# Performance work log

Measured on AMD Instinct MI355X. Metric: run time of the kernel, lower is better.

Reference implementation:

```python
import jax, jax.numpy as jnp
import numpy as np
from jax import lax

# --- model/problem dims (see init_kwargs) ---
G, NPG, R, F, HID, L = 40, 500, 8, 256, 256, 3   # graphs(frames), nodes/graph, relations, feat, hidden, layers
N = G * NPG                                       # 20000 nodes
EPG = 8000
E = G * EPG                                       # 320000 edges
TOTAL = L * HID                                   # 768 = concat of layer outputs
LSTM_IN, LSTM_HID, NCLASS = 256, 256, 2
RATIO = 0.5
K = int(np.ceil(RATIO * NPG))                     # 250 nodes kept per graph by SAGPool


def setup_inputs() -> dict:
    key = jax.random.key(0)
    ks = jax.random.split(key, 16)
    s = 0.05
    x = jax.random.normal(ks[0], (N, F), dtype=jnp.float32)
    # intra-graph edges: node ids offset by graph index
    off = jnp.arange(G, dtype=jnp.int32)[:, None] * NPG
    src = jax.random.randint(ks[1], (G, EPG), 0, NPG, dtype=jnp.int32) + off
    dst = jax.random.randint(ks[2], (G, EPG), 0, NPG, dtype=jnp.int32) + off
    edge_index = jnp.stack([src.reshape(-1), dst.reshape(-1)])
    edge_attr = jax.random.randint(ks[3], (E,), 0, R, dtype=jnp.int32)
    batch = jnp.repeat(jnp.arange(G, dtype=jnp.int32), NPG)
    # RGCN layer params (layer0 in=F==HID so all layers stack)
    conv_W = jax.random.normal(ks[4], (L, R, HID, HID), dtype=jnp.float32) * s
    conv_root = jax.random.normal(ks[5], (L, HID, HID), dtype=jnp.float32) * s
    conv_bias = jnp.zeros((L, HID), dtype=jnp.float32)
    # SAGPool scorer: RGCNConv(TOTAL, 1, R)
    pool_W = jax.random.normal(ks[6], (R, TOTAL, 1), dtype=jnp.float32) * s
    pool_root = jax.random.normal(ks[7], (TOTAL, 1), dtype=jnp.float32) * s
    pool_bias = jnp.zeros((1,), dtype=jnp.float32)
    fc1_W = jax.random.normal(ks[8], (LSTM_IN, TOTAL), dtype=jnp.float32) * s
    fc1_b = jnp.zeros((LSTM_IN,), dtype=jnp.float32)
    W_ih = jax.random.normal(ks[9], (4 * LSTM_HID, LSTM_IN), dtype=jnp.float32) * s
    W_hh = jax.random.normal(ks[10], (4 * LSTM_HID, LSTM_HID), dtype=jnp.float32) * s
    b_ih = jnp.zeros((4 * LSTM_HID,), dtype=jnp.float32)
    b_hh = jnp.zeros((4 * LSTM_HID,), dtype=jnp.float32)
    fc2_W = jax.random.normal(ks[11], (NCLASS, LSTM_HID), dtype=jnp.float32) * s
    fc2_b = jnp.zeros((NCLASS,), dtype=jnp.float32)
    return dict(x=x, edge_index=edge_index, edge_attr=edge_attr, batch=batch,
                conv_W=conv_W, conv_root=conv_root, conv_bias=conv_bias,
                pool_W=pool_W, pool_root=pool_root, pool_bias=pool_bias,
                fc1_W=fc1_W, fc1_b=fc1_b, W_ih=W_ih, W_hh=W_hh, b_ih=b_ih, b_hh=b_hh,
                fc2_W=fc2_W, fc2_b=fc2_b)


def rgcn_conv(x, src, dst, etype, W, root, bias):
    """PyG (Fast)RGCNConv: per-relation mean aggregation summed over relations + root + bias."""
    num_nodes = x.shape[0]
    Rr = W.shape[0]
    h_all = jnp.einsum('ni,rio->rno', x, W)          # [R, N, out] per-relation transform
    msg = h_all[etype, src]                           # [E, out] per-edge message
    seg = dst * Rr + etype                            # (node, relation) segment id
    cnt = jax.ops.segment_sum(jnp.ones((src.shape[0],), x.dtype), seg,
                              num_segments=num_nodes * Rr)
    norm = 1.0 / jnp.maximum(cnt[seg], 1.0)           # per-(dst,rel) mean normalization
    agg = jax.ops.segment_sum(msg * norm[:, None], dst, num_segments=num_nodes)
    return agg + x @ root + bias


def lstm_scan(xs, W_ih, W_hh, b_ih, b_hh):
    """torch.nn.LSTM (single layer, batch=1) over sequence xs [T, in]; torch gate order i,f,g,o."""
    H = W_hh.shape[1]
    def step(carry, xt):
        h, c = carry
        gates = xt @ W_ih.T + h @ W_hh.T + b_ih + b_hh
        i, f, g, o = jnp.split(gates, 4)
        c = jax.nn.sigmoid(f) * c + jax.nn.sigmoid(i) * jnp.tanh(g)
        h = jax.nn.sigmoid(o) * jnp.tanh(c)
        return (h, c), h
    init = (jnp.zeros((H,), xs.dtype), jnp.zeros((H,), xs.dtype))
    (h, c), ys = lax.scan(step, init, xs)
    return ys, h


def reference(x, edge_index, edge_attr, batch,
              conv_W, conv_root, conv_bias,
              pool_W, pool_root, pool_bias,
              fc1_W, fc1_b, W_ih, W_hh, b_ih, b_hh, fc2_W, fc2_b):
    src, dst = edge_index[0], edge_index[1]
    # stacked RGCN layers, outputs concatenated (dropout omitted: eval mode)
    h = x
    outs = []
    for l in range(L):
        h = jax.nn.relu(rgcn_conv(h, src, dst, edge_attr, conv_W[l], conv_root[l], conv_bias[l]))
        outs.append(h)
    xc = jnp.concatenate(outs, axis=-1)               # [N, TOTAL]
    # SAGPool: RGCN scorer -> tanh -> per-graph top-k (batch is contiguous equal-size graphs)
    score = jnp.tanh(rgcn_conv(xc, src, dst, edge_attr, pool_W, pool_root, pool_bias).reshape(-1))
    topv, topi = lax.top_k(score.reshape(G, NPG), K)  # [G, K]
    xg = xc.reshape(G, NPG, TOTAL)
    xsel = jnp.take_along_axis(xg, topi[:, :, None], axis=1) * topv[:, :, None]
    # readout_type='mean': global_mean_pool over kept nodes per graph
    readout = xsel.mean(axis=1)                       # [G, TOTAL]
    h1 = jax.nn.relu(readout @ fc1_W.T + fc1_b)       # [G, LSTM_IN]
    # temporal_type='lstm_last': last hidden state over the G-frame sequence
    _, hlast = lstm_scan(h1, W_ih, W_hh, b_ih, b_hh)  # [LSTM_HID]
    logits = hlast @ fc2_W.T + fc2_b                  # [NCLASS]
    return jax.nn.log_softmax(logits, axis=-1)
```

## Files before the change

### kernel.cpp

```cpp
#include <hip/hip_runtime.h>

typedef unsigned short u16;
typedef short bf8 __attribute__((ext_vector_type(8)));
typedef float f4 __attribute__((ext_vector_type(4)));
typedef _Float16 h2v __attribute__((ext_vector_type(2)));
typedef __fp16 g2v __attribute__((ext_vector_type(2)));
typedef unsigned int u4v __attribute__((ext_vector_type(4)));

#define N_NODES 20000
#define N_EDGES 320000
#define NGRAPH 40
#define NPG 500
#define KTOP 250
#define NSEG (N_NODES * 8)

#define P_CONV_BIAS 0
#define P_POOL_W    768
#define P_POOL_ROOT 6912
#define P_POOL_BIAS 7680
#define P_FC1_W     7688
#define P_FC1_B     204296
#define P_W_IH      204552
#define P_B_IH      466696
#define P_B_HH      467720
#define P_FC2_W     468744
#define P_FC2_B     469256
#define P_TOTAL     469264

__device__ __forceinline__ float b2f(u16 u) {
    union { unsigned int i; float f; } v; v.i = ((unsigned int)u) << 16; return v.f;
}
__device__ __forceinline__ u16 f2b(float f) {
    union { float f; unsigned int i; } v; v.f = f;
    unsigned int x = v.i;
    return (u16)((x + 0x7fffu + ((x >> 16) & 1u)) >> 16);
}
__device__ __forceinline__ float wred(float s) {
    #pragma unroll
    for (int off = 32; off > 0; off >>= 1) s += __shfl_down(s, off);
    return s;
}
__device__ __forceinline__ float fdot2u(unsigned a, unsigned b, float c) {
#if __has_builtin(__builtin_amdgcn_fdot2)
    union { unsigned u; h2v h; } ua, ub; ua.u = a; ub.u = b;
    return __builtin_amdgcn_fdot2(ua.h, ub.h, c, false);
#else
    union { unsigned u; g2v h; } ua, ub; ua.u = a; ub.u = b;
    return c + (float)ua.h[0] * (float)ub.h[0] + (float)ua.h[1] * (float)ub.h[1];
#endif
}
__device__ __forceinline__ unsigned packh2(float a, float b) {
    g2v h = __builtin_amdgcn_cvt_pkrtz(a, b);
    union { g2v h; unsigned u; } v; v.h = h; return v.u;
}

__global__ void k_init(unsigned int* __restrict__ flag, unsigned int* __restrict__ cnt,
                       unsigned int* __restrict__ ctr) {
    int i = blockIdx.x * 256 + threadIdx.x;
    if (i < 64) flag[i] = 0u;
    if (i < NSEG) { cnt[i] = 0u; ctr[i] = 0u; }
}

__global__ void k_detect1(const u16* __restrict__ xr, int n, unsigned int* __restrict__ fb) {
    unsigned int local = 0;
    for (int i = blockIdx.x * 256 + threadIdx.x; i < n; i += 64 * 256) {
        unsigned int u = xr[i];
        if (((u >> 7) & 0xFFu) == 0xFFu) local++;
    }
    local = (unsigned int)wred((float)local);
    if ((threadIdx.x & 63) == 0 && local) atomicAdd(&fb[1], local);
}
__global__ void k_detect2(unsigned int* __restrict__ fb) {
    fb[0] = (fb[1] > 8u) ? 1u : 0u;
}

__device__ __forceinline__ u16 load_cvt(const void* src, size_t i, bool f32) {
    return f32 ? f2b(((const float*)src)[i]) : ((const u16*)src)[i];
}

__global__ void k_cvt_all(const void* conv_bias, const void* pool_W, const void* pool_root,
                          const void* pool_bias, const void* fc1_W, const void* fc1_b,
                          const void* W_ih, const void* b_ih, const void* b_hh,
                          const void* fc2_W, const void* fc2_b,
                          u16* __restrict__ parms, const unsigned int* __restrict__ flag) {
    int i = blockIdx.x * 256 + threadIdx.x;
    if (i >= P_TOTAL) return;
    bool f32 = (*flag != 0u);
    u16 v;
    if      (i < P_CONV_BIAS + 768)    v = load_cvt(conv_bias, i - P_CONV_BIAS, f32);
    else if (i < P_POOL_W + 6144)      v = load_cvt(pool_W,    i - P_POOL_W, f32);
    else if (i < P_POOL_ROOT + 768)    v = load_cvt(pool_root, i - P_POOL_ROOT, f32);
    else if (i < P_POOL_BIAS + 1)      v = load_cvt(pool_bias, i - P_POOL_BIAS, f32);
    else if (i < P_FC1_W && i >= P_POOL_BIAS) return;
    else if (i < P_FC1_W + 196608)     v = load_cvt(fc1_W,    i - P_FC1_W, f32);
    else if (i < P_FC1_B + 256)        v = load_cvt(fc1_b,    i - P_FC1_B, f32);
    else if (i < P_W_IH + 262144)      v = load_cvt(W_ih,     i - P_W_IH, f32);
    else if (i < P_B_IH + 1024)        v = load_cvt(b_ih,     i - P_B_IH, f32);
    else if (i < P_B_HH + 1024)        v = load_cvt(b_hh,     i - P_B_HH, f32);
    else if (i < P_FC2_W + 512)        v = load_cvt(fc2_W,    i - P_FC2_W, f32);
    else if (i < P_FC2_B + 2)          v = load_cvt(fc2_b,    i - P_FC2_B, f32);
    else return;
    parms[i] = v;
}

__global__ void k_stage_x(const void* __restrict__ src, u16* __restrict__ xc,
                          const unsigned int* __restrict__ flag) {
    int i = blockIdx.x * 256 + threadIdx.x;
    if (i >= N_NODES * 256) return;
    u16 v = load_cvt(src, i, *flag != 0u);
    int n = i >> 8, f = i & 255;
    xc[(size_t)n * 768 + 512 + f] = v;
}

__global__ void k_count(const int* __restrict__ dst, const int* __restrict__ et,
                        unsigned int* __restrict__ cnt) {
    int e = blockIdx.x * 256 + threadIdx.x;
    if (e < N_EDGES) {
        unsigned d = (unsigned)dst[e]; if (d >= N_NODES) d = 0;
        unsigned r = (unsigned)et[e] & 7u;
        atomicAdd(&cnt[d * 8 + r], 1u);
    }
}
__global__ void k_inv(const unsigned int* __restrict__ cnt, float* __restrict__ inv, int n) {
    int i = blockIdx.x * 256 + threadIdx.x;
    if (i < n) {
        unsigned int c = cnt[i];
        inv[i] = 1.0f / (float)(c < 1u ? 1u : c);
    }
}

__global__ void k_scan1(const unsigned int* __restrict__ cnt, unsigned int* __restrict__ seg,
                        unsigned int* __restrict__ bsum) {
    __shared__ unsigned int s[256];
    int t = threadIdx.x, i = blockIdx.x * 256 + t;
    unsigned int v = (i < NSEG) ? cnt[i] : 0u;
    s[t] = v;
    __syncthreads();
    for (int off = 1; off < 256; off <<= 1) {
        unsigned int add = (t >= off) ? s[t - off] : 0u;
        __syncthreads();
        s[t] += add;
        __syncthreads();
    }
    if (i < NSEG) seg[i] = s[t] - v;
    if (t == 255) bsum[blockIdx.x] = s[255];
}
__global__ void k_scan2(unsigned int* __restrict__ bsum, int nb) {
    __shared__ unsigned int s[1024];
    int t = threadIdx.x;
    unsigned int v = (t < nb) ? bsum[t] : 0u;
    s[t] = v;
    __syncthreads();
    for (int off = 1; off < 1024; off <<= 1) {
        unsigned int add = (t >= off) ? s[t - off] : 0u;
        __syncthreads();
        s[t] += add;
        __syncthreads();
    }
    if (t < nb) bsum[t] = s[t] - v;
}
__global__ void k_scan3(unsigned int* __restrict__ seg, const unsigned int* __restrict__ bsum) {
    int i = blockIdx.x * 256 + threadIdx.x;
    if (i < NSEG) seg[i] += bsum[i >> 8];
    if (i == 0) seg[NSEG] = N_EDGES;
}
__global__ void k_place(const int* __restrict__ src, const int* __restrict__ dst,
                        const int* __restrict__ et, const unsigned int* __restrict__ seg,
                        unsigned int* __restrict__ ctr, const float* __restrict__ inv,
                        unsigned int* __restrict__ skey, float* __restrict__ sw) {
    int e = blockIdx.x * 256 + threadIdx.x;
    if (e >= N_EDGES) return;
    unsigned s = (unsigned)src[e]; if (s >= N_NODES) s = 0;
    unsigned d = (unsigned)dst[e]; if (d >= N_NODES) d = 0;
    unsigned r = (unsigned)et[e] & 7u;
    unsigned key = d * 8 + r;
    unsigned pos = seg[key] + atomicAdd(&ctr[key], 1u);
    skey[pos] = s;
    sw[pos] = inv[key];
}

__global__ void k_transpose2(const void* __restrict__ conv_W, const void* __restrict__ conv_root,
                             u16* __restrict__ Wt, const unsigned int* __restrict__ flag) {
    int idx = blockIdx.x * 256 + threadIdx.x;
    if (idx >= 3 * 36 * 256 * 64) return;
    bool f32 = (*flag != 0u);
    int kk = idx & 63;
    int n = (idx >> 6) & 255;
    int lc = idx >> 14;
    int l = lc / 36, ck = lc % 36;
    int k = ck * 64 + kk;
    u16 v;
    if (k < 2048) {
        int r = k >> 8, i = k & 255;
        v = load_cvt(conv_W, ((size_t)((l * 8 + r) * 256 + i)) * 256 + n, f32);
    } else {
        int i = k - 2048;
        v = load_cvt(conv_root, ((size_t)(l * 256 + i)) * 256 + n, f32);
    }
    Wt[idx] = v;
}
__global__ void k_whh4(const void* __restrict__ W_hh, unsigned int* __restrict__ whh4,
                       const unsigned int* __restrict__ flag) {
    int idx = blockIdx.x * 256 + threadIdx.x;
    if (idx >= 32 * 1024 * 4) return;
    int c = idx & 3, j = (idx >> 2) & 1023, i4 = idx >> 12;
    int i2 = i4 * 4 + c;
    bool f32 = (*flag != 0u);
    float a, b;
    if (f32) {
        a = ((const float*)W_hh)[j * 256 + 2 * i2];
        b = ((const float*)W_hh)[j * 256 + 2 * i2 + 1];
    } else {
        a = b2f(((const u16*)W_hh)[j * 256 + 2 * i2]);
        b = b2f(((const u16*)W_hh)[j * 256 + 2 * i2 + 1]);
    }
    whh4[idx] = packh2(a, b);
}

__launch_bounds__(256, 4)
__global__ void k_layer(const unsigned int* __restrict__ seg,
                        const unsigned int* __restrict__ skey,
                        const float* __restrict__ sw,
                        const u16* __restrict__ xprev,
                        const u16* __restrict__ WtL,
                        const u16* __restrict__ bias,
                        u16* __restrict__ xc, int colbase) {
    __shared__ u16 As[32 * 264];
    int wave = threadIdx.x >> 6, lane = threadIdx.x & 63;
    int m0 = blockIdx.x * 32;
    int mrow = lane & 15, quad = lane >> 4;
    int nbase = wave * 64;
    int grow = threadIdx.x & 31;
    int ggrp = threadIdx.x >> 5;
    int gm = m0 + grow;
    const u16* gcol = xprev + ggrp * 32;

    f4 acc[4][2];
    #pragma unroll
    for (int nt = 0; nt < 4; ++nt)
        #pragma unroll
        for (int mh = 0; mh < 2; ++mh) acc[nt][mh] = (f4){0.0f, 0.0f, 0.0f, 0.0f};

    for (int rg = 0; rg < 9; ++rg) {
        __syncthreads();
        if (rg < 8) {
            float a[32];
            #pragma unroll
            for (int c = 0; c < 32; ++c) a[c] = 0.0f;
            unsigned nb = seg[gm * 8 + rg], ne = seg[gm * 8 + rg + 1];
            for (unsigned i = nb; i < ne; ++i) {
                float wgt = sw[i];
                const u16* row = gcol + (size_t)skey[i] * 768;
                #pragma unroll
                for (int k8 = 0; k8 < 4; ++k8) {
                    bf8 u = *(const bf8*)(row + k8 * 8);
                    #pragma unroll
                    for (int c = 0; c < 8; ++c)
                        a[k8 * 8 + c] += wgt * b2f((u16)u[c]);
                }
            }
            #pragma unroll
            for (int k8 = 0; k8 < 4; ++k8) {
                bf8 o;
                #pragma unroll
                for (int c = 0; c < 8; ++c) o[c] = (short)f2b(a[k8 * 8 + c]);
                *(bf8*)(As + grow * 264 + ggrp * 32 + k8 * 8) = o;
            }
        } else {
            const u16* row = gcol + (size_t)gm * 768;
            #pragma unroll
            for (int k8 = 0; k8 < 4; ++k8)
                *(bf8*)(As + grow * 264 + ggrp * 32 + k8 * 8) =
                    *(const bf8*)(row + k8 * 8);
        }
        __syncthreads();
        #pragma unroll
        for (int c4 = 0; c4 < 4; ++c4) {
            const u16* Bck = WtL + (size_t)(rg * 4 + c4) * 16384;
            #pragma unroll
            for (int ks = 0; ks < 2; ++ks) {
                bf8 a0 = *(const bf8*)(As + mrow * 264 + c4 * 64 + ks * 32 + quad * 8);
                bf8 a1 = *(const bf8*)(As + (16 + mrow) * 264 + c4 * 64 + ks * 32 + quad * 8);
                #pragma unroll
                for (int nt = 0; nt < 4; ++nt) {
                    bf8 b = *(const bf8*)(Bck + (size_t)(nbase + nt * 16 + mrow) * 64
                                          + ks * 32 + quad * 8);
                    acc[nt][0] = __builtin_amdgcn_mfma_f32_16x16x32_bf16(a0, b, acc[nt][0], 0, 0, 0);
                    acc[nt][1] = __builtin_amdgcn_mfma_f32_16x16x32_bf16(a1, b, acc[nt][1], 0, 0, 0);
                }
            }
        }
    }
    __syncthreads();
    #pragma unroll
    for (int nt = 0; nt < 4; ++nt) {
        int col = nbase + nt * 16 + mrow;
        float bv = b2f(bias[col]);
        #pragma unroll
        for (int mh = 0; mh < 2; ++mh)
            #pragma unroll
            for (int v = 0; v < 4; ++v) {
                float val = acc[nt][mh][v] + bv;
                val = val > 0.0f ? val : 0.0f;
                As[(mh * 16 + quad * 4 + v) * 264 + col] = f2b(val);
            }
    }
    __syncthreads();
    int row = threadIdx.x >> 3;
    int c0 = (threadIdx.x & 7) * 32;
    u16* dst = xc + (size_t)(m0 + row) * 768 + colbase + c0;
    const u16* srcp = As + row * 264 + c0;
    #pragma unroll
    for (int c = 0; c < 4; ++c)
        *(bf8*)(dst + c * 8) = *(const bf8*)(srcp + c * 8);
}

__launch_bounds__(256)
__global__ void k_pool(const u16* __restrict__ xc, const u16* __restrict__ parms,
                       float* __restrict__ p, float* __restrict__ score) {
    int n = blockIdx.x * 4 + (threadIdx.x >> 6);
    if (n >= N_NODES) return;
    int lane = threadIdx.x & 63;
    const u16* xr = xc + (size_t)n * 768;
    float acc[9];
    #pragma unroll
    for (int rr = 0; rr < 9; ++rr) acc[rr] = 0.0f;
    #pragma unroll
    for (int q = 0; q < 12; ++q) {
        int f = lane + 64 * q;
        float xv = b2f(xr[f]);
        #pragma unroll
        for (int rr = 0; rr < 8; ++rr)
            acc[rr] += xv * b2f(parms[P_POOL_W + rr * 768 + f]);
        acc[8] += xv * b2f(parms[P_POOL_ROOT + f]);
    }
    #pragma unroll
    for (int rr = 0; rr < 9; ++rr) acc[rr] = wred(acc[rr]);
    if (lane == 0) {
        #pragma unroll
        for (int rr = 0; rr < 8; ++rr) p[rr * N_NODES + n] = acc[rr];
        score[n] = acc[8] + b2f(parms[P_POOL_BIAS]);
    }
}
__global__ void k_scatter_pool(const int* __restrict__ src, const int* __restrict__ dst,
                               const int* __restrict__ et, const float* __restrict__ inv,
                               const float* __restrict__ p, float* __restrict__ score) {
    int e = blockIdx.x * 256 + threadIdx.x;
    if (e >= N_EDGES) return;
    int r = et[e] & 7;
    unsigned s = (unsigned)src[e]; if (s >= N_NODES) s = 0;
    unsigned d = (unsigned)dst[e]; if (d >= N_NODES) d = 0;
    atomicAdd(&score[d], inv[d * 8 + r] * p[r * N_NODES + s]);
}

__launch_bounds__(256)
__global__ void k_sort(const float* __restrict__ score, unsigned int* __restrict__ topidx,
                       float* __restrict__ topv) {
    __shared__ unsigned long long keys[512];
    __shared__ float vals[512];
    int g = blockIdx.x, tid = threadIdx.x;
    for (int i = tid; i < 512; i += 256) {
        unsigned long long key;
        float v = 0.0f;
        if (i < NPG) {
            v = tanhf(score[g * NPG + i]);
            unsigned int u = __float_as_uint(v);
            u = (u & 0x80000000u) ? ~u : (u | 0x80000000u);
            u = ~u;
            key = ((unsigned long long)u << 32) | (unsigned int)i;
        } else {
            key = 0xFFFFFFFFFFFFFFFFull;
        }
        keys[i] = key;
        vals[i] = v;
    }
    __syncthreads();
    for (int k = 2; k <= 512; k <<= 1)
        for (int j = k >> 1; j > 0; j >>= 1) {
            for (int i = tid; i < 512; i += 256) {
                int ixj = i ^ j;
                if (ixj > i) {
                    bool up = ((i & k) == 0);
                    unsigned long long a = keys[i], b = keys[ixj];
                    if ((a > b) == up) { keys[i] = b; keys[ixj] = a; }
                }
            }
            __syncthreads();
        }
    if (tid < KTOP) {
        int idx = (int)(keys[tid] & 511u);
        topidx[g * 256 + tid] = (unsigned)idx;
        topv[g * 256 + tid] = vals[idx];
    }
}

__launch_bounds__(256)
__global__ void k_readout(const unsigned int* __restrict__ topidx,
                          const float* __restrict__ topv,
                          const u16* __restrict__ xc, float* __restrict__ readout) {
    __shared__ unsigned int sidx[KTOP];
    __shared__ float sv[KTOP];
    __shared__ float part[256];
    int g = blockIdx.x, cb = blockIdx.y;
    int tid = threadIdx.x;
    if (tid < KTOP) { sidx[tid] = topidx[g * 256 + tid]; sv[tid] = topv[g * 256 + tid]; }
    __syncthreads();
    int fl = tid & 63, ng = tid >> 6;
    int f = cb * 64 + fl;
    float acc = 0.0f;
    for (int j = ng; j < KTOP; j += 4)
        acc += sv[j] * b2f(xc[(size_t)(g * NPG + sidx[j]) * 768 + f]);
    part[tid] = acc;
    __syncthreads();
    if (tid < 64) {
        float s = part[tid] + part[64 + tid] + part[128 + tid] + part[192 + tid];
        readout[(size_t)g * 768 + cb * 64 + tid] = s * (1.0f / (float)KTOP);
    }
}

__global__ void k_fc1(const float* __restrict__ readout, const u16* __restrict__ parms,
                      float* __restrict__ h1) {
    int wid = blockIdx.x * 4 + (threadIdx.x >> 6);
    if (wid >= NGRAPH * 256) return;
    int g = wid >> 8, o = wid & 255, lane = threadIdx.x & 63;
    const float* rr = readout + (size_t)g * 768;
    const u16* w = parms + P_FC1_W + (size_t)o * 768;
    float s = 0.0f;
    #pragma unroll
    for (int q = 0; q < 12; ++q) { int f = lane + 64 * q; s += rr[f] * b2f(w[f]); }
    s = wred(s);
    if (lane == 0) { s += b2f(parms[P_FC1_B + o]); h1[g * 256 + o] = s > 0.0f ? s : 0.0f; }
}
__global__ void k_gx(const float* __restrict__ h1, const u16* __restrict__ parms,
                     float* __restrict__ gx) {
    int wid = blockIdx.x * 4 + (threadIdx.x >> 6);
    if (wid >= NGRAPH * 1024) return;
    int t = wid >> 10, j = wid & 1023, lane = threadIdx.x & 63;
    const float* xr = h1 + t * 256;
    const u16* w = parms + P_W_IH + (size_t)j * 256;
    float s = 0.0f;
    #pragma unroll
    for (int q = 0; q < 4; ++q) { int f = lane + 64 * q; s += xr[f] * b2f(w[f]); }
    s = wred(s);
    if (lane == 0) gx[t * 1024 + j] = s + b2f(parms[P_B_IH + j]) + b2f(parms[P_B_HH + j]);
}

__launch_bounds__(512, 2)
__global__ void k_lstm(const float* __restrict__ gx, const unsigned int* __restrict__ whh4,
                       const u16* __restrict__ parms, void* __restrict__ out,
                       const unsigned int* __restrict__ flag) {
    __shared__ float hs[256];
    __shared__ unsigned int hs2[128];
    __shared__ float gs[1024];
    __shared__ float red[2];
    int tid = threadIdx.x;
    int j0 = tid, j1 = tid + 512;
    u4v wa[24], wb[24];
    #pragma unroll
    for (int q = 0; q < 24; ++q) {
        wa[q] = *(const u4v*)(whh4 + (((size_t)q * 1024) + j0) * 4);
        wb[q] = *(const u4v*)(whh4 + (((size_t)q * 1024) + j1) * 4);
    }
    asm volatile("" : "+v"(wa[0]), "+v"(wa[1]), "+v"(wa[2]), "+v"(wa[3]),
                      "+v"(wa[4]), "+v"(wa[5]), "+v"(wa[6]), "+v"(wa[7]),
                      "+v"(wa[8]), "+v"(wa[9]), "+v"(wa[10]), "+v"(wa[11]),
                      "+v"(wa[12]), "+v"(wa[13]), "+v"(wa[14]), "+v"(wa[15]),
                      "+v"(wa[16]), "+v"(wa[17]), "+v"(wa[18]), "+v"(wa[19]),
                      "+v"(wa[20]), "+v"(wa[21]), "+v"(wa[22]), "+v"(wa[23]));
    asm volatile("" : "+v"(wb[0]), "+v"(wb[1]), "+v"(wb[2]), "+v"(wb[3]),
                      "+v"(wb[4]), "+v"(wb[5]), "+v"(wb[6]), "+v"(wb[7]),
                      "+v"(wb[8]), "+v"(wb[9]), "+v"(wb[10]), "+v"(wb[11]),
                      "+v"(wb[12]), "+v"(wb[13]), "+v"(wb[14]), "+v"(wb[15]),
                      "+v"(wb[16]), "+v"(wb[17]), "+v"(wb[18]), "+v"(wb[19]),
                      "+v"(wb[20]), "+v"(wb[21]), "+v"(wb[22]), "+v"(wb[23]));
    if (tid < 256) hs[tid] = 0.0f;
    if (tid < 128) hs2[tid] = 0u;
    float c = 0.0f;
    __syncthreads();
    for (int t = 0; t < NGRAPH; ++t) {
        float g0 = gx[t * 1024 + j0];
        float g1 = gx[t * 1024 + j1];
        #pragma unroll
        for (int q = 0; q < 24; ++q) {
            #pragma unroll
            for (int cc = 0; cc < 4; ++cc) {
                unsigned h2 = hs2[q * 4 + cc];
                g0 = fdot2u(wa[q][cc], h2, g0);
                g1 = fdot2u(wb[q][cc], h2, g1);
            }
        }
        #pragma unroll 4
        for (int q = 24; q < 32; ++q) {
            u4v v0 = *(const u4v*)(whh4 + (((size_t)q * 1024) + j0) * 4);
            u4v v1 = *(const u4v*)(whh4 + (((size_t)q * 1024) + j1) * 4);
            #pragma unroll
            for (int cc = 0; cc < 4; ++cc) {
                unsigned h2 = hs2[q * 4 + cc];
                g0 = fdot2u(v0[cc], h2, g0);
                g1 = fdot2u(v1[cc], h2, g1);
            }
        }
        gs[j0] = g0;
        gs[j1] = g1;
        __syncthreads();
        if (tid < 256) {
            float gi = 1.0f / (1.0f + expf(-gs[tid]));
            float gf = 1.0f / (1.0f + expf(-gs[256 + tid]));
            float gg = tanhf(gs[512 + tid]);
            float go = 1.0f / (1.0f + expf(-gs[768 + tid]));
            c = gf * c + gi * gg;
            float h = go * tanhf(c);
            hs[tid] = h;
            float ho = __shfl(h, (tid & 63) ^ 1);
            if (!(tid & 1)) hs2[tid >> 1] = packh2(h, ho);
        }
        __syncthreads();
    }
    if (tid < 128) {
        int cls = tid >> 6, lane = tid & 63;
        float s = 0.0f;
        #pragma unroll
        for (int q = 0; q < 4; ++q) {
            int d = lane + 64 * q;
            s += hs[d] * b2f(parms[P_FC2_W + cls * 256 + d]);
        }
        s = wred(s);
        if (lane == 0) red[cls] = s + b2f(parms[P_FC2_B + cls]);
    }
    __syncthreads();
    if (tid == 0) {
        float l0 = red[0], l1 = red[1];
        float m = fmaxf(l0, l1);
        float lse = m + logf(expf(l0 - m) + expf(l1 - m));
        float o0 = l0 - lse, o1 = l1 - lse;
        if (*flag) { ((float*)out)[0] = o0; ((float*)out)[1] = o1; }
        else       { ((u16*)out)[0] = f2b(o0); ((u16*)out)[1] = f2b(o1); }
    }
}

struct WS {
    unsigned int* flag; unsigned int* cnt; float* inv; unsigned int* seg; unsigned int* ctr;
    unsigned int* skey; float* sw; unsigned int* bsum;
    u16* Wt2; u16* xc; float* p; float* score;
    unsigned int* topidx; float* topv;
    float* readout; float* h1; float* gx; unsigned int* whh4; u16* parms;
    size_t need;
};
static WS plan(char* base) {
    WS w; size_t off = 0;
    auto take = [&](size_t bytes) -> char* {
        char* p = base + off; off += (bytes + 255) & ~(size_t)255; return p;
    };
    w.flag    = (unsigned int*)take(256);
    w.cnt     = (unsigned int*)take((size_t)NSEG * 4);
    w.inv     = (float*)take((size_t)NSEG * 4);
    w.seg     = (unsigned int*)take((size_t)(NSEG + 1) * 4);
    w.ctr     = (unsigned int*)take((size_t)NSEG * 4);
    w.skey    = (unsigned int*)take((size_t)N_EDGES * 4);
    w.sw      = (float*)take((size_t)N_EDGES * 4);
    w.bsum    = (unsigned int*)take(1024 * 4);
    w.Wt2     = (u16*)take((size_t)3 * 36 * 256 * 64 * 2);
    w.xc      = (u16*)take((size_t)N_NODES * 768 * 2);
    w.p       = (float*)take((size_t)8 * N_NODES * 4);
    w.score   = (float*)take((size_t)N_NODES * 4);
    w.topidx  = (unsigned int*)take((size_t)NGRAPH * 256 * 4);
    w.topv    = (float*)take((size_t)NGRAPH * 256 * 4);
    w.readout = (float*)take((size_t)NGRAPH * 768 * 4);
    w.h1      = (float*)take((size_t)NGRAPH * 256 * 4);
    w.gx      = (float*)take((size_t)NGRAPH * 1024 * 4);
    w.whh4    = (unsigned int*)take((size_t)32 * 1024 * 4 * 4);
    w.parms   = (u16*)take((size_t)P_TOTAL * 2);
    w.need = off;
    return w;
}

extern "C" void kernel_launch(void* const* d_in, const int* in_sizes, int n_in,
                              void* d_out, int out_size, void* d_ws, size_t ws_size,
                              hipStream_t stream) {
    (void)in_sizes; (void)n_in; (void)out_size; (void)ws_size;
    const void* x        = d_in[0];
    const int* edge_index= (const int*)d_in[1];
    const int* edge_attr = (const int*)d_in[2];
    const void* conv_W   = d_in[4];
    const void* conv_root= d_in[5];
    const void* conv_bias= d_in[6];
    const void* pool_W   = d_in[7];
    const void* pool_root= d_in[8];
    const void* pool_bias= d_in[9];
    const void* fc1_W    = d_in[10];
    const void* fc1_b    = d_in[11];
    const void* W_ih     = d_in[12];
    const void* W_hh     = d_in[13];
    const void* b_ih     = d_in[14];
    const void* b_hh     = d_in[15];
    const void* fc2_W    = d_in[16];
    const void* fc2_b    = d_in[17];

    const int* e_src = edge_index;
    const int* e_dst = edge_index + N_EDGES;

    WS w = plan((char*)d_ws);

    k_init<<<(NSEG + 255) / 256, 256, 0, stream>>>(w.flag, w.cnt, w.ctr);
    k_detect1<<<64, 256, 0, stream>>>((const u16*)x, 1 << 18, w.flag);
    k_detect2<<<1, 1, 0, stream>>>(w.flag);

    k_count<<<1250, 256, 0, stream>>>(e_dst, edge_attr, w.cnt);
    k_inv<<<(NSEG + 255) / 256, 256, 0, stream>>>(w.cnt, w.inv, NSEG);
    k_scan1<<<625, 256, 0, stream>>>(w.cnt, w.seg, w.bsum);
    k_scan2<<<1, 1024, 0, stream>>>(w.bsum, 625);
    k_scan3<<<(NSEG + 255) / 256, 256, 0, stream>>>(w.seg, w.bsum);
    k_place<<<1250, 256, 0, stream>>>(e_src, e_dst, edge_attr, w.seg, w.ctr, w.inv,
                                      w.skey, w.sw);

    k_cvt_all<<<(P_TOTAL + 255) / 256, 256, 0, stream>>>(
        conv_bias, pool_W, pool_root, pool_bias, fc1_W, fc1_b,
        W_ih, b_ih, b_hh, fc2_W, fc2_b, w.parms, w.flag);

    k_stage_x<<<20000, 256, 0, stream>>>(x, w.xc, w.flag);
    k_transpose2<<<6912, 256, 0, stream>>>(conv_W, conv_root, w.Wt2, w.flag);
    k_whh4<<<512, 256, 0, stream>>>(W_hh, w.whh4, w.flag);

    for (int l = 0; l < 3; ++l) {
        const u16* xprev = w.xc + (l == 0 ? 512 : (l - 1) * 256);
        const u16* WtL = w.Wt2 + (size_t)l * 36 * 16384;
        const u16* bias = w.parms + P_CONV_BIAS + l * 256;
        k_layer<<<625, 256, 0, stream>>>(w.seg, w.skey, w.sw, xprev, WtL, bias,
                                         w.xc, l * 256);
    }

    k_pool<<<5000, 256, 0, stream>>>(w.xc, w.parms, w.p, w.score);
    k_scatter_pool<<<1250, 256, 0, stream>>>(e_src, e_dst, edge_attr, w.inv, w.p, w.score);
    k_sort<<<NGRAPH, 256, 0, stream>>>(w.score, w.topidx, w.topv);
    k_readout<<<dim3(NGRAPH, 12), 256, 0, stream>>>(w.topidx, w.topv, w.xc, w.readout);
    k_fc1<<<2560, 256, 0, stream>>>(w.readout, w.parms, w.h1);
    k_gx<<<10240, 256, 0, stream>>>(w.h1, w.parms, w.gx);
    k_lstm<<<1, 512, 0, stream>>>(w.gx, w.whh4, w.parms, d_out, w.flag);
}
```

Baseline: 792.1 us.

## Reorder RGCN to transform-then-aggregate with per-relation GEMM and edge gather

Instead of aggregating neighbor features per relation and then multiplying by W_r, each layer first computes H_r = X·W_r for all 8 relations plus root into a workspace buffer with a dense MFMA GEMM, then a gather kernel sums weighted rows of H over each node's edges, adding root, bias and ReLU. Edge keys now encode the relation and a chunk-local source index so nodes can be processed in chunks sized to the available workspace. This removes the scattered per-edge aggregation interleaved with the GEMM, at the cost of a large intermediate write/read (9×N×256 bf16) and, if workspace is small, many more launches. Rounding H to bf16 before aggregation also changes numerics slightly.

```diff
diff --git a/kernel.cpp b/kernel.cpp
--- a/kernel.cpp
+++ b/kernel.cpp
@@ -2,6 +2,7 @@
 
 typedef unsigned short u16;
 typedef short bf8 __attribute__((ext_vector_type(8)));
+typedef short bf4 __attribute__((ext_vector_type(4)));
 typedef float f4 __attribute__((ext_vector_type(4)));
 typedef _Float16 h2v __attribute__((ext_vector_type(2)));
 typedef __fp16 g2v __attribute__((ext_vector_type(2)));
@@ -167,7 +168,7 @@
 __global__ void k_place(const int* __restrict__ src, const int* __restrict__ dst,
                         const int* __restrict__ et, const unsigned int* __restrict__ seg,
                         unsigned int* __restrict__ ctr, const float* __restrict__ inv,
-                        unsigned int* __restrict__ skey, float* __restrict__ sw) {
+                        unsigned int* __restrict__ skey, float* __restrict__ sw, int chn) {
     int e = blockIdx.x * 256 + threadIdx.x;
     if (e >= N_EDGES) return;
     unsigned s = (unsigned)src[e]; if (s >= N_NODES) s = 0;
@@ -175,7 +176,10 @@
     unsigned r = (unsigned)et[e] & 7u;
     unsigned key = d * 8 + r;
     unsigned pos = seg[key] + atomicAdd(&ctr[key], 1u);
-    skey[pos] = s;
+    unsigned base = (d / (unsigned)chn) * (unsigned)chn;
+    unsigned sl = s - base;
+    if (sl >= (unsigned)chn) sl = 0u;
+    skey[pos] = sl | (r << 16);
     sw[pos] = inv[key];
 }
 
@@ -217,102 +221,124 @@
     whh4[idx] = packh2(a, b);
 }
 
-__launch_bounds__(256, 4)
-__global__ void k_layer(const unsigned int* __restrict__ seg,
-                        const unsigned int* __restrict__ skey,
-                        const float* __restrict__ sw,
-                        const u16* __restrict__ xprev,
-                        const u16* __restrict__ WtL,
-                        const u16* __restrict__ bias,
-                        u16* __restrict__ xc, int colbase) {
-    __shared__ u16 As[32 * 264];
+__launch_bounds__(256, 3)
+__global__ void k_layer2(const u16* __restrict__ xprev,
+                         const u16* __restrict__ WtL,
+                         u16* __restrict__ Hall, int n0, int chn) {
+    __shared__ u16 As[64 * 264];
+    int m0 = n0 + blockIdx.x * 64;
+    int rg = blockIdx.y;
+    int nend = n0 + chn;
     int wave = threadIdx.x >> 6, lane = threadIdx.x & 63;
-    int m0 = blockIdx.x * 32;
     int mrow = lane & 15, quad = lane >> 4;
     int nbase = wave * 64;
-    int grow = threadIdx.x & 31;
-    int ggrp = threadIdx.x >> 5;
-    int gm = m0 + grow;
-    const u16* gcol = xprev + ggrp * 32;
-
-    f4 acc[4][2];
+
+    {
+        int row = threadIdx.x >> 2, sg = threadIdx.x & 3;
+        int gm = m0 + row;
+        u16* dstp = As + row * 264 + sg * 64;
+        if (gm < nend) {
+            const u16* srcp = xprev + (size_t)gm * 768 + sg * 64;
+            #pragma unroll
+            for (int c = 0; c < 8; ++c)
+                *(bf8*)(dstp + c * 8) = *(const bf8*)(srcp + c * 8);
+        } else {
+            bf8 z = {0, 0, 0, 0, 0, 0, 0, 0};
+            #pragma unroll
+            for (int c = 0; c < 8; ++c) *(bf8*)(dstp + c * 8) = z;
+        }
+    }
+    __syncthreads();
+
+    f4 acc[4][4];
     #pragma unroll
     for (int nt = 0; nt < 4; ++nt)
         #pragma unroll
-        for (int mh = 0; mh < 2; ++mh) acc[nt][mh] = (f4){0.0f, 0.0f, 0.0f, 0.0f};
-
-    for (int rg = 0; rg < 9; ++rg) {
-        __syncthreads();
-        if (rg < 8) {
-            float a[32];
-            #pragma unroll
-            for (int c = 0; c < 32; ++c) a[c] = 0.0f;
-            unsigned nb = seg[gm * 8 + rg], ne = seg[gm * 8 + rg + 1];
-            for (unsigned i = nb; i < ne; ++i) {
-                float wgt = sw[i];
-                const u16* row = gcol + (size_t)skey[i] * 768;
+        for (int mh = 0; mh < 4; ++mh) acc[nt][mh] = (f4){0.0f, 0.0f, 0.0f, 0.0f};
+
+    const u16* WtR = WtL + (size_t)(rg * 4) * 16384;
+    #pragma unroll
+    for (int c4 = 0; c4 < 4; ++c4) {
+        const u16* Bck = WtR + (size_t)c4 * 16384;
+        #pragma unroll
+        for (int ks = 0; ks < 2; ++ks) {
+            bf8 a[4];
+            #pragma unroll
+            for (int mh = 0; mh < 4; ++mh)
+                a[mh] = *(const bf8*)(As + (mh * 16 + mrow) * 264 + c4 * 64 + ks * 32 + quad * 8);
+            #pragma unroll
+            for (int nt = 0; nt < 4; ++nt) {
+                bf8 b = *(const bf8*)(Bck + (size_t)(nbase + nt * 16 + mrow) * 64
+                                      + ks * 32 + quad * 8);
                 #pragma unroll
-                for (int k8 = 0; k8 < 4; ++k8) {
-                    bf8 u = *(const bf8*)(row + k8 * 8);
-                    #pragma unroll
-                    for (int c = 0; c < 8; ++c)
-                        a[k8 * 8 + c] += wgt * b2f((u16)u[c]);
-                }
+                for (int mh = 0; mh < 4; ++mh)
+                    acc[nt][mh] = __builtin_amdgcn_mfma_f32_16x16x32_bf16(a[mh], b, acc[nt][mh], 0, 0, 0);
             }
-            #pragma unroll
-            for (int k8 = 0; k8 < 4; ++k8) {
-                bf8 o;
-                #pragma unroll
-                for (int c = 0; c < 8; ++c) o[c] = (short)f2b(a[k8 * 8 + c]);
-                *(bf8*)(As + grow * 264 + ggrp * 32 + k8 * 8) = o;
-            }
-        } else {
-            const u16* row = gcol + (size_t)gm * 768;
-            #pragma unroll
-            for (int k8 = 0; k8 < 4; ++k8)
-                *(bf8*)(As + grow * 264 + ggrp * 32 + k8 * 8) =
-                    *(const bf8*)(row + k8 * 8);
-        }
-        __syncthreads();
-        #pragma unroll
-        for (int c4 = 0; c4 < 4; ++c4) {
-            const u16* Bck = WtL + (size_t)(rg * 4 + c4) * 16384;
-            #pragma unroll
-            for (int ks = 0; ks < 2; ++ks) {
-                bf8 a0 = *(const bf8*)(As + mrow * 264 + c4 * 64 + ks * 32 + quad * 8);
-                bf8 a1 = *(const bf8*)(As + (16 + mrow) * 264 + c4 * 64 + ks * 32 + quad * 8);
-                #pragma unroll
-                for (int nt = 0; nt < 4; ++nt) {
-                    bf8 b = *(const bf8*)(Bck + (size_t)(nbase + nt * 16 + mrow) * 64
-                                          + ks * 32 + quad * 8);
-                    acc[nt][0] = __builtin_amdgcn_mfma_f32_16x16x32_bf16(a0, b, acc[nt][0], 0, 0, 0);
-                    acc[nt][1] = __builtin_amdgcn_mfma_f32_16x16x32_bf16(a1, b, acc[nt][1], 0, 0, 0);
-                }
-            }
-        }
-    }
+        }
+    }
+
     __syncthreads();
     #pragma unroll
     for (int nt = 0; nt < 4; ++nt) {
         int col = nbase + nt * 16 + mrow;
-        float bv = b2f(bias[col]);
         #pragma unroll
-        for (int mh = 0; mh < 2; ++mh)
-            #pragma unroll
-            for (int v = 0; v < 4; ++v) {
-                float val = acc[nt][mh][v] + bv;
-                val = val > 0.0f ? val : 0.0f;
-                As[(mh * 16 + quad * 4 + v) * 264 + col] = f2b(val);
-            }
-    }
-    __syncthreads();
-    int row = threadIdx.x >> 3;
-    int c0 = (threadIdx.x & 7) * 32;
-    u16* dst = xc + (size_t)(m0 + row) * 768 + colbase + c0;
-    const u16* srcp = As + row * 264 + c0;
-    #pragma unroll
-    for (int c = 0; c < 4; ++c)
-        *(bf8*)(dst + c * 8) = *(const bf8*)(srcp + c * 8);
+        for (int mh = 0; mh < 4; ++mh)
+            #pragma unroll
+            for (int v = 0; v < 4; ++v)
+                As[(mh * 16 + quad * 4 + v) * 264 + col] = f2b(acc[nt][mh][v]);
+    }
+    __syncthreads();
+    {
+        int row = threadIdx.x >> 2, sg = threadIdx.x & 3;
+        int gm = m0 + row;
+        if (gm < nend) {
+            u16* dst = Hall + ((size_t)rg * chn + (gm - n0)) * 256 + sg * 64;
+            const u16* srcp = As + row * 264 + sg * 64;
+            #pragma unroll
+            for (int c = 0; c < 8; ++c)
+                *(bf8*)(dst + c * 8) = *(const bf8*)(srcp + c * 8);
+        }
+    }
+}
+
+__launch_bounds__(256)
+__global__ void k_gather(const unsigned int* __restrict__ seg,
+                         const unsigned int* __restrict__ skey,
+                         const float* __restrict__ sw,
+                         const u16* __restrict__ Hall,
+                         const u16* __restrict__ bias,
+                         u16* __restrict__ xc, int colbase, int n0, int chn) {
+    int nl = blockIdx.x * 4 + (threadIdx.x >> 6);
+    int n = n0 + nl;
+    int lane = threadIdx.x & 63;
+    int c0 = lane * 4;
+    unsigned e0 = seg[n * 8], e1 = seg[n * 8 + 8];
+    float a0 = 0.0f, a1 = 0.0f, a2 = 0.0f, a3 = 0.0f;
+    unsigned key = 0; float w = 0.0f;
+    if (e0 < e1) { key = skey[e0]; w = sw[e0]; }
+    for (unsigned e = e0; e < e1;) {
+        unsigned kc = key; float wc = w;
+        ++e;
+        if (e < e1) { key = skey[e]; w = sw[e]; }
+        const u16* row = Hall + ((size_t)(kc >> 16) * chn + (kc & 0xFFFFu)) * 256 + c0;
+        bf4 v = *(const bf4*)row;
+        a0 += wc * b2f((u16)v[0]);
+        a1 += wc * b2f((u16)v[1]);
+        a2 += wc * b2f((u16)v[2]);
+        a3 += wc * b2f((u16)v[3]);
+    }
+    const u16* rr = Hall + ((size_t)8 * chn + nl) * 256 + c0;
+    bf4 rv = *(const bf4*)rr;
+    float o0 = a0 + b2f((u16)rv[0]) + b2f(bias[c0 + 0]);
+    float o1 = a1 + b2f((u16)rv[1]) + b2f(bias[c0 + 1]);
+    float o2 = a2 + b2f((u16)rv[2]) + b2f(bias[c0 + 2]);
+    float o3 = a3 + b2f((u16)rv[3]) + b2f(bias[c0 + 3]);
+    bf4 o;
+    o[0] = (short)f2b(o0 > 0.0f ? o0 : 0.0f);
+    o[1] = (short)f2b(o1 > 0.0f ? o1 : 0.0f);
+    o[2] = (short)f2b(o2 > 0.0f ? o2 : 0.0f);
+    o[3] = (short)f2b(o3 > 0.0f ? o3 : 0.0f);
+    *(bf4*)(xc + (size_t)n * 768 + colbase + c0) = o;
 }
 
 __launch_bounds__(256)
@@ -541,12 +567,12 @@
 struct WS {
     unsigned int* flag; unsigned int* cnt; float* inv; unsigned int* seg; unsigned int* ctr;
     unsigned int* skey; float* sw; unsigned int* bsum;
-    u16* Wt2; u16* xc; float* p; float* score;
+    u16* Wt2; u16* xc; u16* Hall; float* p; float* score;
     unsigned int* topidx; float* topv;
     float* readout; float* h1; float* gx; unsigned int* whh4; u16* parms;
     size_t need;
 };
-static WS plan(char* base) {
+static WS plan(char* base, int chn) {
     WS w; size_t off = 0;
     auto take = [&](size_t bytes) -> char* {
         char* p = base + off; off += (bytes + 255) & ~(size_t)255; return p;
@@ -561,6 +587,7 @@
     w.bsum    = (unsigned int*)take(1024 * 4);
     w.Wt2     = (u16*)take((size_t)3 * 36 * 256 * 64 * 2);
     w.xc      = (u16*)take((size_t)N_NODES * 768 * 2);
+    w.Hall    = (u16*)take((size_t)9 * chn * 256 * 2);
     w.p       = (float*)take((size_t)8 * N_NODES * 4);
     w.score   = (float*)take((size_t)N_NODES * 4);
     w.topidx  = (unsigned int*)take((size_t)NGRAPH * 256 * 4);
@@ -577,7 +604,7 @@
 extern "C" void kernel_launch(void* const* d_in, const int* in_sizes, int n_in,
                               void* d_out, int out_size, void* d_ws, size_t ws_size,
                               hipStream_t stream) {
-    (void)in_sizes; (void)n_in; (void)out_size; (void)ws_size;
+    (void)in_sizes; (void)n_in; (void)out_size;
     const void* x        = d_in[0];
     const int* edge_index= (const int*)d_in[1];
     const int* edge_attr = (const int*)d_in[2];
@@ -599,7 +626,15 @@
     const int* e_src = edge_index;
     const int* e_dst = edge_index + N_EDGES;
 
-    WS w = plan((char*)d_ws);
+    if (ws_size == 0) ws_size = (size_t)64 << 20;
+    int chn = 500;
+    {
+        const int ladder[4] = {20000, 4000, 1000, 500};
+        for (int i = 0; i < 4; ++i) {
+            if (plan((char*)d_ws, ladder[i]).need <= ws_size) { chn = ladder[i]; break; }
+        }
+    }
+    WS w = plan((char*)d_ws, chn);
 
     k_init<<<(NSEG + 255) / 256, 256, 0, stream>>>(w.flag, w.cnt, w.ctr);
     k_detect1<<<64, 256, 0, stream>>>((const u16*)x, 1 << 18, w.flag);
@@ -611,7 +646,7 @@
     k_scan2<<<1, 1024, 0, stream>>>(w.bsum, 625);
     k_scan3<<<(NSEG + 255) / 256, 256, 0, stream>>>(w.seg, w.bsum);
     k_place<<<1250, 256, 0, stream>>>(e_src, e_dst, edge_attr, w.seg, w.ctr, w.inv,
-                                      w.skey, w.sw);
+                                      w.skey, w.sw, chn);
 
     k_cvt_all<<<(P_TOTAL + 255) / 256, 256, 0, stream>>>(
         conv_bias, pool_W, pool_root, pool_bias, fc1_W, fc1_b,
@@ -621,12 +656,18 @@
     k_transpose2<<<6912, 256, 0, stream>>>(conv_W, conv_root, w.Wt2, w.flag);
     k_whh4<<<512, 256, 0, stream>>>(W_hh, w.whh4, w.flag);
 
+    int nch = N_NODES / chn;
+    int gx_tiles = (chn + 63) / 64;
     for (int l = 0; l < 3; ++l) {
         const u16* xprev = w.xc + (l == 0 ? 512 : (l - 1) * 256);
         const u16* WtL = w.Wt2 + (size_t)l * 36 * 16384;
         const u16* bias = w.parms + P_CONV_BIAS + l * 256;
-        k_layer<<<625, 256, 0, stream>>>(w.seg, w.skey, w.sw, xprev, WtL, bias,
-                                         w.xc, l * 256);
+        for (int c = 0; c < nch; ++c) {
+            int n0 = c * chn;
+            k_layer2<<<dim3(gx_tiles, 9), 256, 0, stream>>>(xprev, WtL, w.Hall, n0, chn);
+            k_gather<<<chn / 4, 256, 0, stream>>>(w.seg, w.skey, w.sw, w.Hall, bias,
+                                                  w.xc, l * 256, n0, chn);
+        }
     }
 
     k_pool<<<5000, 256, 0, stream>>>(w.xc, w.parms, w.p, w.score);
```

New measurement: 705.3 us. 1.12x faster.
